# Kernel tuning notes

Hardware: AMD Instinct MI355X
Metric: run time of the kernel (lower is better)

Reference implementation:

```python
import jax, jax.numpy as jnp
import numpy as np

LORA_RANK = 16
LORA_ALPHA = 16
LORA_SCALE = LORA_ALPHA / LORA_RANK


def setup_inputs() -> dict:
    key = jax.random.key(0)
    k1, k2, k3, k4, k5 = jax.random.split(key, 5)
    B, S, D_IN, D_OUT, N_LORA, R = 8, 2048, 4096, 4096, 3, LORA_RANK
    std = 1.0 / np.sqrt(D_IN)
    x = jax.random.normal(k1, (B, S, D_IN), dtype=jnp.float32)
    weight = jax.random.truncated_normal(k2, -3.0, 3.0, (D_OUT, D_IN), dtype=jnp.float32) * std
    bias = jax.random.normal(k3, (D_OUT,), dtype=jnp.float32) * 0.01
    lora_A = jax.random.normal(k4, (N_LORA, R, D_IN), dtype=jnp.float32) * std
    lora_B = jax.random.normal(k5, (N_LORA, D_OUT, R), dtype=jnp.float32) * 0.02
    # segment starts: samples 0-1 -> no LoRA (index 0 reserved), 2-3 -> adapter 1, 4-5 -> adapter 2, 6-7 -> adapter 3
    lora_start_indices = jnp.arange(4, dtype=jnp.int64) * 2
    return {"x": x, "weight": weight, "bias": bias, "lora_A": lora_A,
            "lora_B": lora_B, "lora_start_indices": lora_start_indices}


def reference(x, weight, bias, lora_A, lora_B, lora_start_indices):
    # Base linear: y = x @ W^T + b   (torch: weight @ x_column)
    y = jnp.einsum('bsd,od->bso', x, weight) + bias  # [B,S,D_out]
    B = x.shape[0]
    # Map each batch sample to its segment (SGMV-style dispatch over contiguous segments).
    seg = jnp.searchsorted(lora_start_indices, jnp.arange(B), side='right') - 1  # [B], 0 = no LoRA
    adapter_idx = jnp.clip(seg - 1, 0, lora_A.shape[0] - 1)
    A = lora_A[adapter_idx]   # [B, r, D_in]  (tiny gather)
    Bw = lora_B[adapter_idx]  # [B, D_out, r]
    lo = jnp.einsum('bsr,bor->bso', jnp.einsum('bsd,brd->bsr', x, A), Bw) * LORA_SCALE
    use_lora = (seg > 0)[:, None, None]
    return y + jnp.where(use_lora, lo, jnp.zeros((), dtype=y.dtype))
```

## Files before the change

kernel.cpp:

```cpp
#include <hip/hip_runtime.h>


typedef __attribute__((ext_vector_type(8))) short short8;
typedef __attribute__((ext_vector_type(4))) float f32x4;
typedef __attribute__((ext_vector_type(4))) unsigned short u16x4;
typedef unsigned short u16;

typedef __attribute__((address_space(1))) void as1_void;
typedef __attribute__((address_space(3))) void as3_void;

#define M_DIM 16384
#define N_DIM 4096
#define K_DIM 4096

__device__ __forceinline__ u16 f2bf(float f) {
  union { float f; unsigned u; } v; v.f = f;
  unsigned r = (v.u + 0x7FFFu + ((v.u >> 16) & 1u)) >> 16;
  return (u16)r;
}
__device__ __forceinline__ float bf2f(u16 u) {
  union { unsigned u; float f; } v; v.u = ((unsigned)u) << 16;
  return v.f;
}
__device__ __forceinline__ void gload16(const void* g, void* lds) {
  __builtin_amdgcn_global_load_lds((as1_void*)g, (as3_void*)lds, 16, 0, 0);
}
__device__ __forceinline__ int seg_of_batch(const int* starts, int b) {
  int seg = -1;
#pragma unroll
  for (int i = 0; i < 4; ++i) seg += (starts[i] <= b) ? 1 : 0;
  return seg;
}

__global__ __launch_bounds__(256) void prep_kernel(
    const float* __restrict__ x, const float* __restrict__ wgt,
    const float* __restrict__ lA, const float* __restrict__ lB,
    u16* __restrict__ xbf, u16* __restrict__ wbf,
    u16* __restrict__ abf, u16* __restrict__ bw) {
  const long long NX4 = 16777216LL;
  const long long NW4 = 4194304LL;
  const long long NA4 = 49152LL;
  const long long NB  = 12288LL;
  const long long total = NX4 + NW4 + NA4 + NB;
  const f32x4* x4 = (const f32x4*)x;
  const f32x4* w4 = (const f32x4*)wgt;
  const f32x4* a4 = (const f32x4*)lA;
  u16x4* xo = (u16x4*)xbf;
  u16x4* wo = (u16x4*)wbf;
  u16x4* ao = (u16x4*)abf;
  for (long long i = (long long)blockIdx.x * blockDim.x + threadIdx.x; i < total;
       i += (long long)gridDim.x * blockDim.x) {
    if (i < NX4) {
      f32x4 v = x4[i];
      u16x4 o = {f2bf(v.x), f2bf(v.y), f2bf(v.z), f2bf(v.w)};
      xo[i] = o;
    } else if (i < NX4 + NW4) {
      long long j = i - NX4;
      f32x4 v = w4[j];
      u16x4 o = {f2bf(v.x), f2bf(v.y), f2bf(v.z), f2bf(v.w)};
      wo[j] = o;
    } else if (i < NX4 + NW4 + NA4) {
      long long j = i - NX4 - NW4;
      f32x4 v = a4[j];
      u16x4 o = {f2bf(v.x), f2bf(v.y), f2bf(v.z), f2bf(v.w)};
      ao[j] = o;
    } else {
      long long p = i - NX4 - NW4 - NA4;
      const float* src = lB + p * 16;
      u16* dst = bw + p * 32;
#pragma unroll
      for (int j = 0; j < 16; ++j) dst[j] = f2bf(src[j]);
#pragma unroll
      for (int j = 16; j < 32; ++j) dst[j] = 0;
    }
  }
}

__global__ __launch_bounds__(256) void ucompute_kernel(
    const u16* __restrict__ xbf, const u16* __restrict__ abf,
    const int* __restrict__ starts, u16* __restrict__ u) {
  const int l = threadIdx.x & 63;
  const int w = threadIdx.x >> 6;
  const int mbase = blockIdx.x * 16 + w * 4;
  const int b = mbase >> 11;
  const int seg = seg_of_batch(starts, b);
  const int use = seg > 0;
  int ad = seg - 1; ad = ad < 0 ? 0 : (ad > 2 ? 2 : ad);

  float acc[4][16];
#pragma unroll
  for (int row = 0; row < 4; ++row)
#pragma unroll
    for (int r = 0; r < 16; ++r) acc[row][r] = 0.f;

  if (use) {
    const u16* xr = xbf + (size_t)mbase * K_DIM + l * 8;
    const u16* ar = abf + (size_t)ad * (16 * K_DIM) + l * 8;
    for (int pass = 0; pass < 8; ++pass) {
      const int off = pass * 512;
      float xv[4][8];
#pragma unroll
      for (int row = 0; row < 4; ++row) {
        short8 xs = *(const short8*)(xr + (size_t)row * K_DIM + off);
#pragma unroll
        for (int j = 0; j < 8; ++j) xv[row][j] = bf2f((u16)xs[j]);
      }
#pragma unroll
      for (int r = 0; r < 16; ++r) {
        short8 av = *(const short8*)(ar + (size_t)r * K_DIM + off);
#pragma unroll
        for (int j = 0; j < 8; ++j) {
          float a = bf2f((u16)av[j]);
#pragma unroll
          for (int row = 0; row < 4; ++row) acc[row][r] += xv[row][j] * a;
        }
      }
    }
  }
#pragma unroll
  for (int row = 0; row < 4; ++row) {
    float myval = 0.f;
#pragma unroll
    for (int r = 0; r < 16; ++r) {
      float v = acc[row][r];
      v += __shfl_xor(v, 32);
      v += __shfl_xor(v, 16);
      v += __shfl_xor(v, 8);
      v += __shfl_xor(v, 4);
      v += __shfl_xor(v, 2);
      v += __shfl_xor(v, 1);
      if (l == r) myval = v;
    }
    if (l < 32) u[(size_t)(mbase + row) * 32 + l] = (l < 16) ? f2bf(myval) : (u16)0;
  }
}

__device__ __forceinline__ void do_tile(const u16* ard, const u16* brd,
                                        f32x4 (&acc)[4][4]) {
  short8 af[4], bf_[4];
#pragma unroll
  for (int i = 0; i < 4; ++i) af[i] = *(const short8*)(ard + i * 512);
#pragma unroll
  for (int j = 0; j < 4; ++j) bf_[j] = *(const short8*)(brd + j * 512);
#pragma unroll
  for (int i = 0; i < 4; ++i)
#pragma unroll
    for (int j = 0; j < 4; ++j)
      acc[i][j] = __builtin_amdgcn_mfma_f32_16x16x32_bf16(af[i], bf_[j], acc[i][j], 0, 0, 0);
}

__global__ __launch_bounds__(256) void gemm_kernel(
    const u16* __restrict__ xbf, const u16* __restrict__ wbf,
    const float* __restrict__ bias, const u16* __restrict__ ubuf,
    const u16* __restrict__ bwpad, const int* __restrict__ starts,
    float* __restrict__ out) {
  __shared__ u16 As[128 * 32];
  __shared__ u16 Bs[128 * 32];

  const int tid = threadIdx.x;
  const int l = tid & 63;
  const int w = tid >> 6;
  const int m0 = blockIdx.y << 7;
  const int n0 = blockIdx.x << 7;

  const int b = m0 >> 11;
  const int seg = seg_of_batch(starts, b);
  int ad = seg - 1; ad = ad < 0 ? 0 : (ad > 2 ? 2 : ad);

  const int srow = l >> 2;
  const int scolb = (l & 3) << 4;
  const int reg0 = w * 2;
  const int r0row = reg0 * 16 + srow;
  const int r1row = (reg0 + 1) * 16 + srow;

  const char* a0 = (const char*)(xbf + (size_t)(m0 + r0row) * K_DIM) + scolb;
  const char* a1 = (const char*)(xbf + (size_t)(m0 + r1row) * K_DIM) + scolb;
  const char* b0 = (const char*)(wbf + (size_t)(n0 + r0row) * K_DIM) + scolb;
  const char* b1 = (const char*)(wbf + (size_t)(n0 + r1row) * K_DIM) + scolb;

  u16* lda0 = As + reg0 * 512;
  u16* lda1 = As + (reg0 + 1) * 512;
  u16* ldb0 = Bs + reg0 * 512;
  u16* ldb1 = Bs + (reg0 + 1) * 512;

  const int fm = l & 15;
  const int fk = (l >> 4) << 3;
  const int wr = w >> 1, wc = w & 1;
  const u16* ard = As + (size_t)(wr * 64 + fm) * 32 + fk;
  const u16* brd = Bs + (size_t)(wc * 64 + fm) * 32 + fk;

  f32x4 acc[4][4];
  const f32x4 z4 = {0.f, 0.f, 0.f, 0.f};
#pragma unroll
  for (int i = 0; i < 4; ++i)
#pragma unroll
    for (int j = 0; j < 4; ++j) acc[i][j] = z4;

  for (int kt = 0; kt < 128; ++kt) {
    const size_t off = (size_t)kt << 6;
    gload16(a0 + off, lda0);
    gload16(a1 + off, lda1);
    gload16(b0 + off, ldb0);
    gload16(b1 + off, ldb1);
    __syncthreads();
    do_tile(ard, brd, acc);
    __syncthreads();
  }
  gload16((const char*)(ubuf + (size_t)(m0 + r0row) * 32) + scolb, lda0);
  gload16((const char*)(ubuf + (size_t)(m0 + r1row) * 32) + scolb, lda1);
  gload16((const char*)(bwpad + ((size_t)ad * N_DIM + n0 + r0row) * 32) + scolb, ldb0);
  gload16((const char*)(bwpad + ((size_t)ad * N_DIM + n0 + r1row) * 32) + scolb, ldb1);
  __syncthreads();
  do_tile(ard, brd, acc);

  float bv[4];
#pragma unroll
  for (int j = 0; j < 4; ++j) bv[j] = bias[n0 + wc * 64 + j * 16 + fm];
  const int q = l >> 4;
#pragma unroll
  for (int i = 0; i < 4; ++i) {
#pragma unroll
    for (int ii = 0; ii < 4; ++ii) {
      const int m = m0 + wr * 64 + i * 16 + q * 4 + ii;
      float* orow = out + (size_t)m * N_DIM + n0 + wc * 64 + fm;
#pragma unroll
      for (int j = 0; j < 4; ++j) orow[j * 16] = acc[i][j][ii] + bv[j];
    }
  }
}

__global__ __launch_bounds__(256) void u_f32_kernel(
    const float* __restrict__ x, const float* __restrict__ lA,
    const int* __restrict__ starts, float* __restrict__ u) {
  const int l = threadIdx.x & 63;
  const int w = threadIdx.x >> 6;
  const int m = blockIdx.x * 4 + w;
  const int b = m >> 11;
  const int seg = seg_of_batch(starts, b);
  const int use = seg > 0;
  int ad = seg - 1; ad = ad < 0 ? 0 : (ad > 2 ? 2 : ad);
  float acc[16];
#pragma unroll
  for (int r = 0; r < 16; ++r) acc[r] = 0.f;
  if (use) {
    const float* xr = x + (size_t)m * K_DIM + l * 4;
    const float* ar = lA + (size_t)ad * (16 * K_DIM) + l * 4;
    for (int pass = 0; pass < 16; ++pass) {
      const int off = pass * 256;
      f32x4 xv = *(const f32x4*)(xr + off);
#pragma unroll
      for (int r = 0; r < 16; ++r) {
        f32x4 av = *(const f32x4*)(ar + (size_t)r * K_DIM + off);
        acc[r] += xv.x * av.x + xv.y * av.y + xv.z * av.z + xv.w * av.w;
      }
    }
  }
  float myval = 0.f;
#pragma unroll
  for (int r = 0; r < 16; ++r) {
    float v = acc[r];
    v += __shfl_xor(v, 32);
    v += __shfl_xor(v, 16);
    v += __shfl_xor(v, 8);
    v += __shfl_xor(v, 4);
    v += __shfl_xor(v, 2);
    v += __shfl_xor(v, 1);
    if (l == r) myval = v;
  }
  if (l < 16) u[(size_t)m * 16 + l] = myval;
}

__global__ __launch_bounds__(256) void gemm_f32_fallback(
    const float* __restrict__ x, const float* __restrict__ wgt,
    const float* __restrict__ bias, const float* __restrict__ lB,
    const float* __restrict__ u, const int* __restrict__ starts,
    float* __restrict__ out) {
  __shared__ float xs[4096];
  const int m = blockIdx.y;
  const int n0 = blockIdx.x * 256;
  const int t = threadIdx.x;
  const f32x4* xr4 = (const f32x4*)(x + (size_t)m * K_DIM);
  f32x4* xs4 = (f32x4*)xs;
  for (int i = t; i < 1024; i += 256) xs4[i] = xr4[i];
  __syncthreads();
  const int b = m >> 11;
  const int seg = seg_of_batch(starts, b);
  const int use = seg > 0;
  int ad = seg - 1; ad = ad < 0 ? 0 : (ad > 2 ? 2 : ad);
  const int n = n0 + t;
  const f32x4* wr = (const f32x4*)(wgt + (size_t)n * K_DIM);
  float acc = 0.f;
  for (int kk = 0; kk < 1024; ++kk) {
    f32x4 wv = wr[kk];
    f32x4 xv = xs4[kk];
    acc += xv.x * wv.x + xv.y * wv.y + xv.z * wv.z + xv.w * wv.w;
  }
  acc += bias[n];
  if (use) {
    const float* Bn = lB + ((size_t)ad * N_DIM + n) * 16;
    const float* um = u + (size_t)m * 16;
    float lo = 0.f;
#pragma unroll
    for (int r = 0; r < 16; ++r) lo += um[r] * Bn[r];
    acc += lo;
  }
  out[(size_t)m * N_DIM + n] = acc;
}

extern "C" void kernel_launch(void* const* d_in, const int* in_sizes, int n_in,
                              void* d_out, int out_size, void* d_ws, size_t ws_size,
                              hipStream_t stream) {
  const float* x    = (const float*)d_in[0];
  const float* wgt  = (const float*)d_in[1];
  const float* bias = (const float*)d_in[2];
  const float* lA   = (const float*)d_in[3];
  const float* lB   = (const float*)d_in[4];
  const int* starts = (const int*)d_in[5];
  float* out = (float*)d_out;

  const size_t XBF_OFF = 0;
  const size_t WBF_OFF = 134217728;
  const size_t ABF_OFF = 167772160;
  const size_t BW_OFF  = 168165376;
  const size_t U_OFF   = 168951808;
  const size_t WS_NEEDED = 170000384;

  if (ws_size >= WS_NEEDED) {
    u16* xbf = (u16*)((char*)d_ws + XBF_OFF);
    u16* wbf = (u16*)((char*)d_ws + WBF_OFF);
    u16* abf = (u16*)((char*)d_ws + ABF_OFF);
    u16* bw  = (u16*)((char*)d_ws + BW_OFF);
    u16* u   = (u16*)((char*)d_ws + U_OFF);
    prep_kernel<<<8192, 256, 0, stream>>>(x, wgt, lA, lB, xbf, wbf, abf, bw);
    ucompute_kernel<<<1024, 256, 0, stream>>>(xbf, abf, starts, u);
    gemm_kernel<<<dim3(32, 128), 256, 0, stream>>>(xbf, wbf, bias, u, bw, starts, out);
  } else {
    float* uf = (float*)d_ws;
    u_f32_kernel<<<4096, 256, 0, stream>>>(x, lA, starts, uf);
    gemm_f32_fallback<<<dim3(16, 16384), 256, 0, stream>>>(x, wgt, bias, lB, uf, starts, out);
  }
}
```

Baseline: 1.328 ms.

## Rewrite bf16 GEMM with 256x256 double-buffered swizzled tiles and XCD block remap

Replaces the 128x128, BK=32, single-buffered GEMM with a 512-thread kernel that computes 256x256 output tiles with BK=64. It double-buffers LDS through direct global-to-LDS loads, interleaved into eight compute phases with explicit vmcnt waits and raised priority around the MFMA blocks. LDS addresses are XOR-swizzled to avoid bank conflicts, and block IDs are remapped so neighbouring tiles share cache. The larger tiles cut global traffic per FLOP and overlap loads with compute, but they raise register and LDS pressure and limit occupancy to one block per CU.

```diff
diff --git a/kernel.cpp b/kernel.cpp
--- a/kernel.cpp
+++ b/kernel.cpp
@@ -12,6 +12,10 @@
 #define M_DIM 16384
 #define N_DIM 4096
 #define K_DIM 4096
+#define K2 8192
+#define BM 256
+#define BN 256
+#define BK 64
 
 __device__ __forceinline__ u16 f2bf(float f) {
   union { float f; unsigned u; } v; v.f = f;
@@ -31,6 +35,8 @@
   for (int i = 0; i < 4; ++i) seg += (starts[i] <= b) ? 1 : 0;
   return seg;
 }
+
+#define VMCNT(n) asm volatile("s_waitcnt vmcnt(" #n ")" ::: "memory")
 
 __global__ __launch_bounds__(256) void prep_kernel(
     const float* __restrict__ x, const float* __restrict__ wgt,
@@ -135,93 +141,153 @@
   }
 }
 
-__device__ __forceinline__ void do_tile(const u16* ard, const u16* brd,
-                                        f32x4 (&acc)[4][4]) {
-  short8 af[4], bf_[4];
-#pragma unroll
-  for (int i = 0; i < 4; ++i) af[i] = *(const short8*)(ard + i * 512);
-#pragma unroll
-  for (int j = 0; j < 4; ++j) bf_[j] = *(const short8*)(brd + j * 512);
-#pragma unroll
-  for (int i = 0; i < 4; ++i)
-#pragma unroll
-    for (int j = 0; j < 4; ++j)
-      acc[i][j] = __builtin_amdgcn_mfma_f32_16x16x32_bf16(af[i], bf_[j], acc[i][j], 0, 0, 0);
-}
-
-__global__ __launch_bounds__(256) void gemm_kernel(
+
+#define STAGE_A(buf, ih, kt) do { \
+  gload16(aSrc + (size_t)((ih)*64) * K2 + (size_t)(kt)*128, \
+          &As[buf][((ih)*64) * BK] + w * 512); \
+  gload16(aSrc + (size_t)((ih)*64 + 128) * K2 + (size_t)(kt)*128, \
+          &As[buf][((ih)*64 + 128) * BK] + w * 512); \
+} while (0)
+#define STAGE_B(buf, jh, kt) do { \
+  gload16(bSrc + (size_t)((jh)*32) * K2 + (size_t)(kt)*128, \
+          &Bs[buf][((jh)*32 + (w >> 2)*64) * BK] + (w & 3) * 512); \
+  gload16(bSrc + (size_t)((jh)*32 + 128) * K2 + (size_t)(kt)*128, \
+          &Bs[buf][((jh)*32 + (w >> 2)*64 + 128) * BK] + (w & 3) * 512); \
+} while (0)
+
+#define PHASE(buf, ih, jh, STAGE_STMT, WAIT_STMT) do { \
+  short8 aF0[4], aF1[4], bF0[2], bF1[2]; \
+  _Pragma("unroll") \
+  for (int i2 = 0; i2 < 4; ++i2) { \
+    const u16* ar = &As[buf][(wr*128 + (ih)*64 + i2*16 + fm) * BK]; \
+    aF0[i2] = *(const short8*)(ar + c0); \
+    aF1[i2] = *(const short8*)(ar + c1); \
+  } \
+  _Pragma("unroll") \
+  for (int j2 = 0; j2 < 2; ++j2) { \
+    const u16* br = &Bs[buf][(wc*64 + (jh)*32 + j2*16 + fm) * BK]; \
+    bF0[j2] = *(const short8*)(br + c0); \
+    bF1[j2] = *(const short8*)(br + c1); \
+  } \
+  STAGE_STMT; \
+  WAIT_STMT; \
+  __builtin_amdgcn_s_barrier(); \
+  __builtin_amdgcn_s_setprio(1); \
+  _Pragma("unroll") \
+  for (int i2 = 0; i2 < 4; ++i2) \
+  _Pragma("unroll") \
+  for (int j2 = 0; j2 < 2; ++j2) { \
+    acc[(ih)*4 + i2][(jh)*2 + j2] = __builtin_amdgcn_mfma_f32_16x16x32_bf16( \
+        aF0[i2], bF0[j2], acc[(ih)*4 + i2][(jh)*2 + j2], 0, 0, 0); \
+    acc[(ih)*4 + i2][(jh)*2 + j2] = __builtin_amdgcn_mfma_f32_16x16x32_bf16( \
+        aF1[i2], bF1[j2], acc[(ih)*4 + i2][(jh)*2 + j2], 0, 0, 0); \
+  } \
+  __builtin_amdgcn_s_setprio(0); \
+  __builtin_amdgcn_s_barrier(); \
+} while (0)
+
+__global__ __launch_bounds__(512, 2) void gemm8_kernel(
     const u16* __restrict__ xbf, const u16* __restrict__ wbf,
     const float* __restrict__ bias, const u16* __restrict__ ubuf,
     const u16* __restrict__ bwpad, const int* __restrict__ starts,
     float* __restrict__ out) {
-  __shared__ u16 As[128 * 32];
-  __shared__ u16 Bs[128 * 32];
+  __shared__ u16 As[2][BM * BK];
+  __shared__ u16 Bs[2][BN * BK];
 
   const int tid = threadIdx.x;
   const int l = tid & 63;
   const int w = tid >> 6;
-  const int m0 = blockIdx.y << 7;
-  const int n0 = blockIdx.x << 7;
+
+  const int bid = blockIdx.x;
+  const int nb = (bid & 7) * 128 + (bid >> 3);
+  const int m0 = (nb >> 4) << 8;
+  const int n0 = (nb & 15) << 8;
 
   const int b = m0 >> 11;
   const int seg = seg_of_batch(starts, b);
   int ad = seg - 1; ad = ad < 0 ? 0 : (ad > 2 ? 2 : ad);
 
-  const int srow = l >> 2;
-  const int scolb = (l & 3) << 4;
-  const int reg0 = w * 2;
-  const int r0row = reg0 * 16 + srow;
-  const int r1row = (reg0 + 1) * 16 + srow;
-
-  const char* a0 = (const char*)(xbf + (size_t)(m0 + r0row) * K_DIM) + scolb;
-  const char* a1 = (const char*)(xbf + (size_t)(m0 + r1row) * K_DIM) + scolb;
-  const char* b0 = (const char*)(wbf + (size_t)(n0 + r0row) * K_DIM) + scolb;
-  const char* b1 = (const char*)(wbf + (size_t)(n0 + r1row) * K_DIM) + scolb;
-
-  u16* lda0 = As + reg0 * 512;
-  u16* lda1 = As + (reg0 + 1) * 512;
-  u16* ldb0 = Bs + reg0 * 512;
-  u16* ldb1 = Bs + (reg0 + 1) * 512;
+  const int lrow = l >> 3;
+  const int swzslot = (l & 7) ^ lrow;
+  const char* aSrc = (const char*)xbf +
+      (size_t)(m0 + 8 * w + lrow) * K2 + swzslot * 16;
+  const char* bSrc = (const char*)wbf +
+      (size_t)(n0 + (w >> 2) * 64 + (w & 3) * 8 + lrow) * K2 + swzslot * 16;
 
   const int fm = l & 15;
-  const int fk = (l >> 4) << 3;
-  const int wr = w >> 1, wc = w & 1;
-  const u16* ard = As + (size_t)(wr * 64 + fm) * 32 + fk;
-  const u16* brd = Bs + (size_t)(wc * 64 + fm) * 32 + fk;
-
-  f32x4 acc[4][4];
+  const int q = l >> 4;
+  const int wr = w >> 2;
+  const int wc = w & 3;
+  const int c0 = ((q ^ (fm & 7)) * 8);
+  const int c1 = (((q + 4) ^ (fm & 7)) * 8);
+
+  f32x4 acc[8][4];
   const f32x4 z4 = {0.f, 0.f, 0.f, 0.f};
 #pragma unroll
-  for (int i = 0; i < 4; ++i)
+  for (int i = 0; i < 8; ++i)
 #pragma unroll
     for (int j = 0; j < 4; ++j) acc[i][j] = z4;
 
-  for (int kt = 0; kt < 128; ++kt) {
-    const size_t off = (size_t)kt << 6;
-    gload16(a0 + off, lda0);
-    gload16(a1 + off, lda1);
-    gload16(b0 + off, ldb0);
-    gload16(b1 + off, ldb1);
-    __syncthreads();
-    do_tile(ard, brd, acc);
-    __syncthreads();
-  }
-  gload16((const char*)(ubuf + (size_t)(m0 + r0row) * 32) + scolb, lda0);
-  gload16((const char*)(ubuf + (size_t)(m0 + r1row) * 32) + scolb, lda1);
-  gload16((const char*)(bwpad + ((size_t)ad * N_DIM + n0 + r0row) * 32) + scolb, ldb0);
-  gload16((const char*)(bwpad + ((size_t)ad * N_DIM + n0 + r1row) * 32) + scolb, ldb1);
-  __syncthreads();
-  do_tile(ard, brd, acc);
+  STAGE_A(0, 0, 0); STAGE_B(0, 0, 0); STAGE_A(0, 1, 0); STAGE_B(0, 1, 0);
+  STAGE_A(1, 0, 1); STAGE_B(1, 0, 1);
+  VMCNT(4);
+  __builtin_amdgcn_s_barrier();
+
+  for (int s = 0; s < 32; ++s) {
+    const int t1 = 2 * s + 1;
+    const int t2 = 2 * s + 2;
+    const int t3 = 2 * s + 3;
+    const bool more = (s < 31);
+    PHASE(0, 0, 0, STAGE_A(1, 1, t1), (void)0);
+    PHASE(0, 0, 1, STAGE_B(1, 1, t1), (void)0);
+    PHASE(0, 1, 0, if (more) STAGE_A(0, 0, t2), (void)0);
+    PHASE(0, 1, 1, if (more) STAGE_B(0, 0, t2),
+          if (more) VMCNT(4); else VMCNT(0));
+    PHASE(1, 0, 0, if (more) STAGE_A(0, 1, t2), (void)0);
+    PHASE(1, 0, 1, if (more) STAGE_B(0, 1, t2), (void)0);
+    PHASE(1, 1, 0, if (more) STAGE_A(1, 0, t3), (void)0);
+    PHASE(1, 1, 1, if (more) STAGE_B(1, 0, t3),
+          if (more) VMCNT(4); else VMCNT(0));
+  }
+
+  {
+    u16* la = &As[0][0];
+    u16* lb = &Bs[0][0];
+    const int ls = l & 3;
+    const int lr = l >> 2;
+    const char* uSrc = (const char*)ubuf +
+        (size_t)(m0 + 16 * w + lr) * 64 + ls * 16;
+    const char* vSrc = (const char*)bwpad +
+        ((size_t)ad * N_DIM + n0 + 16 * w + lr) * 64 + ls * 16;
+    gload16(uSrc, la + (16 * w) * 32);
+    gload16(uSrc + (size_t)128 * 64, la + (128 + 16 * w) * 32);
+    gload16(vSrc, lb + (16 * w) * 32);
+    gload16(vSrc + (size_t)128 * 64, lb + (128 + 16 * w) * 32);
+    VMCNT(0);
+    __builtin_amdgcn_s_barrier();
+    short8 aF[8], bF[4];
+#pragma unroll
+    for (int i = 0; i < 8; ++i)
+      aF[i] = *(const short8*)(la + (wr * 128 + i * 16 + fm) * 32 + q * 8);
+#pragma unroll
+    for (int j = 0; j < 4; ++j)
+      bF[j] = *(const short8*)(lb + (wc * 64 + j * 16 + fm) * 32 + q * 8);
+#pragma unroll
+    for (int i = 0; i < 8; ++i)
+#pragma unroll
+      for (int j = 0; j < 4; ++j)
+        acc[i][j] = __builtin_amdgcn_mfma_f32_16x16x32_bf16(aF[i], bF[j],
+                                                            acc[i][j], 0, 0, 0);
+  }
 
   float bv[4];
 #pragma unroll
   for (int j = 0; j < 4; ++j) bv[j] = bias[n0 + wc * 64 + j * 16 + fm];
-  const int q = l >> 4;
-#pragma unroll
-  for (int i = 0; i < 4; ++i) {
+#pragma unroll
+  for (int i = 0; i < 8; ++i) {
 #pragma unroll
     for (int ii = 0; ii < 4; ++ii) {
-      const int m = m0 + wr * 64 + i * 16 + q * 4 + ii;
+      const int m = m0 + wr * 128 + i * 16 + q * 4 + ii;
       float* orow = out + (size_t)m * N_DIM + n0 + wc * 64 + fm;
 #pragma unroll
       for (int j = 0; j < 4; ++j) orow[j * 16] = acc[i][j][ii] + bv[j];
@@ -333,7 +399,7 @@
     u16* u   = (u16*)((char*)d_ws + U_OFF);
     prep_kernel<<<8192, 256, 0, stream>>>(x, wgt, lA, lB, xbf, wbf, abf, bw);
     ucompute_kernel<<<1024, 256, 0, stream>>>(xbf, abf, starts, u);
-    gemm_kernel<<<dim3(32, 128), 256, 0, stream>>>(xbf, wbf, bias, u, bw, starts, out);
+    gemm8_kernel<<<1024, 512, 0, stream>>>(xbf, wbf, bias, u, bw, starts, out);
   } else {
     float* uf = (float*)d_ws;
     u_f32_kernel<<<4096, 256, 0, stream>>>(x, lA, starts, uf);
```

After: 1.187 ms. 1.12x faster.
